# Optimization experiments

Hardware: AMD Instinct MI355X
Metric: run time of the kernel (lower is better)

The kernel has to match this reference:

```python
import jax, jax.numpy as jnp
import numpy as np
from jax import lax

T, B, C = 1024, 64, 512


def setup_inputs() -> dict:
    key = jax.random.key(0)
    ks = jax.random.split(key, 9)
    x = jax.random.normal(ks[0], (T, B, C), dtype=jnp.float32)
    reset = jax.random.uniform(ks[1], (T, B)) < 0.05
    h0 = jax.random.normal(ks[2], (1, B, C), dtype=jnp.float32)
    c0 = jax.random.normal(ks[3], (1, B, C), dtype=jnp.float32)
    s = 1.0 / np.sqrt(C)
    W_ih = jax.random.uniform(ks[4], (4 * C, C), minval=-s, maxval=s, dtype=jnp.float32)
    W_hh = jax.random.uniform(ks[5], (4 * C, C), minval=-s, maxval=s, dtype=jnp.float32)
    b_ih = jax.random.uniform(ks[6], (4 * C,), minval=-s, maxval=s, dtype=jnp.float32)
    b_hh = jax.random.uniform(ks[7], (4 * C,), minval=-s, maxval=s, dtype=jnp.float32)
    return {"x": x, "reset": reset, "h0": h0, "c0": c0,
            "W_ih": W_ih, "W_hh": W_hh, "b_ih": b_ih, "b_hh": b_hh}


def _reset_lstm(x, reset, h0, c0, W_ih, W_hh, b_ih, b_hh):
    # Semantics of Packer + cuDNN LSTM: at each step t, (h,c) are zeroed for
    # batch elements with reset[t]=True (including t=0), then a standard LSTM
    # cell (torch gate order i,f,g,o) is applied.
    # Precompute input projections for all steps: [T,B,4C]
    xg = jnp.einsum('tbc,gc->tbg', x, W_ih) + b_ih + b_hh

    def step(carry, inp):
        h, c = carry                      # [B,C]
        xgt, rt = inp                     # [B,4C], [B]
        keep = jnp.logical_not(rt)[:, None].astype(h.dtype)
        h = h * keep
        c = c * keep
        gates = xgt + h @ W_hh.T          # [B,4C]
        i, f, g, o = jnp.split(gates, 4, axis=-1)
        c = jax.nn.sigmoid(f) * c + jax.nn.sigmoid(i) * jnp.tanh(g)
        h = jax.nn.sigmoid(o) * jnp.tanh(c)
        return (h, c), h

    (hn, cn), ys = lax.scan(step, (h0[0], c0[0]), (xg, reset))
    return ys  # [T,B,C]; module's forward returns y only


def reference(x, reset, h0, c0, W_ih, W_hh, b_ih, b_hh):
    return _reset_lstm(x, reset, h0, c0, W_ih, W_hh, b_ih, b_hh)
```

## Files before the change

### kernel.cpp

```cpp
#include <hip/hip_runtime.h>
#include <math.h>

typedef __attribute__((ext_vector_type(8))) short short8;
typedef __attribute__((ext_vector_type(4))) float f32x4;

#define TSTEPS 1024
#define BATCH  64
#define CDIM   512
#define CAP    256
#define NPH    4

#define HEXW_OFF   0
#define HEXW_BYTES ((size_t)16 * NPH * CAP * 512 * 4)
#define GSEG_OFF   (HEXW_OFF + HEXW_BYTES)
#define GSEG_BYTES ((size_t)65536 * 4)
#define GCNT_OFF   (GSEG_OFF + GSEG_BYTES)
#define GCNT_BYTES (1024 * 4)
#define FLG_OFF    (GCNT_OFF + GCNT_BYTES)
#define FLG_BYTES  (256 * 16 * 4)
#define SEGT_OFF   (FLG_OFF + FLG_BYTES)
#define SEGT_BYTES ((size_t)64 * 1024 * 4)
#define WS_NEED    (SEGT_OFF + SEGT_BYTES)

#define SMEM_BYTES 103424

__device__ __forceinline__ unsigned short f2bf(float x) {
  unsigned u = __builtin_bit_cast(unsigned, x);
  unsigned r = (u + 0x7FFFu + ((u >> 16) & 1u)) >> 16;
  return (unsigned short)r;
}
__device__ __forceinline__ short8 pack8(float4 lo, float4 hi) {
  short8 r;
  r[0] = (short)f2bf(lo.x); r[1] = (short)f2bf(lo.y);
  r[2] = (short)f2bf(lo.z); r[3] = (short)f2bf(lo.w);
  r[4] = (short)f2bf(hi.x); r[5] = (short)f2bf(hi.y);
  r[6] = (short)f2bf(hi.z); r[7] = (short)f2bf(hi.w);
  return r;
}
__device__ __forceinline__ float sigm(float z) { return 1.0f / (1.0f + __expf(-z)); }
__device__ __forceinline__ float tanh_f(float x) {
  return 2.0f / (1.0f + __expf(-2.0f * x)) - 1.0f;
}
__device__ __forceinline__ void backoff(int rnd) {
  if (rnd == 1) __builtin_amdgcn_s_sleep(1);
  else if (rnd == 2) __builtin_amdgcn_s_sleep(2);
  else if (rnd == 3) __builtin_amdgcn_s_sleep(4);
  else if (rnd >= 4) __builtin_amdgcn_s_sleep(8);
}

__device__ __forceinline__ void pollg(const unsigned* flg, int g, int cg,
                                      unsigned tgt, int lane) {
  const int idx = lane & 15;
  int rnd = 0;
  while (true) {
    unsigned v = (idx == cg)
                     ? 0xffffffffu
                     : __hip_atomic_load(&flg[(g * 16 + idx) * 16],
                                         __ATOMIC_RELAXED, __HIP_MEMORY_SCOPE_AGENT);
    if (__all((int)(v >= tgt))) break;
    backoff(++rnd > 8 ? 8 : rnd);
  }
  asm volatile("" ::: "memory");
}

__global__ __launch_bounds__(512) void seg_setup(const void* __restrict__ rst,
    unsigned* __restrict__ GSEG, unsigned* __restrict__ GCNT,
    unsigned* __restrict__ SEGT) {
  __shared__ unsigned long long RM[1024];
  __shared__ unsigned long long BM[64][17];
  __shared__ unsigned hist[1025], GCl[1025], cur[1025];
  __shared__ unsigned nsegb[64];
  __shared__ int s_oki, s_okf, s_oddnz;
  const int tid = threadIdx.x, lane = tid & 63, wv = tid >> 6;
  if (tid == 0) { s_oki = 1; s_okf = 1; s_oddnz = 0; }
  __syncthreads();
  {
    int oki = 1, okf = 1, oddnz = 0;
    for (int i = tid; i < 1024; i += 512) {
      unsigned v = ((const unsigned*)rst)[i];
      oki &= (v <= 1u);
      okf &= (v == 0u || v == 0x3F800000u);
      if ((i & 1) && v != 0u) oddnz = 1;
    }
    if (!oki) atomicAnd(&s_oki, 0);
    if (!okf) atomicAnd(&s_okf, 0);
    if (oddnz) atomicOr(&s_oddnz, 1);
  }
  __syncthreads();
  const int mode = s_oki ? (s_oddnz ? 0 : 3) : (s_okf ? 2 : 1);
  for (int tt = wv; tt < 1024; tt += 8) {
    int idx = tt * BATCH + lane;
    bool r;
    if (mode == 0)      r = ((const int*)rst)[idx] != 0;
    else if (mode == 1) r = ((const unsigned char*)rst)[idx] != 0;
    else if (mode == 2) r = ((const float*)rst)[idx] != 0.0f;
    else                r = ((const int*)rst)[2 * idx] != 0;
    unsigned long long bm = __ballot((int)r);
    if (lane == 0) RM[tt] = bm;
  }
  for (int i = tid; i < 1025; i += 512) { hist[i] = 0; cur[i] = 0; }
  __syncthreads();
  for (int idx = wv; idx < 1024; idx += 8) {
    int b = idx >> 4, w = idx & 15;
    unsigned long long bit = (RM[w * 64 + lane] >> b) & 1ull;
    unsigned long long m = __ballot((int)(bit != 0ull));
    if (lane == 0) BM[b][w] = m;
  }
  __syncthreads();
  if (tid < 64) {
    int b = tid; unsigned cnt = 0; int s = 0;
    unsigned seed0 = (BM[b][0] & 1ull) ? 0u : 1u;
    for (int w = 0; w < 16; ++w) {
      unsigned long long m = BM[b][w];
      if (w == 0) m &= ~1ull;
      while (m) {
        int t = w * 64 + __builtin_ctzll(m);
        m &= m - 1;
        unsigned len = (unsigned)(t - s);
        unsigned sd = (s == 0) ? seed0 : 0u;
        SEGT[b * 1024 + cnt++] =
            (len << 17) | ((unsigned)s << 7) | ((unsigned)b << 1) | sd;
        atomicAdd(&hist[len], 1u);
        s = t;
      }
    }
    { unsigned len = (unsigned)(1024 - s);
      unsigned sd = (s == 0) ? seed0 : 0u;
      SEGT[b * 1024 + cnt++] =
          (len << 17) | ((unsigned)s << 7) | ((unsigned)b << 1) | sd;
      atomicAdd(&hist[len], 1u); }
    nsegb[b] = cnt;
  }
  __syncthreads();
  if (tid == 0) {
    unsigned acc = 0;
    for (int r = 1023; r >= 0; --r) { acc += hist[r + 1]; GCl[r] = acc; }
    GCl[1024] = 0;
  }
  __syncthreads();
  if (tid < 64) {
    int b = tid;
    for (unsigned k = 0; k < nsegb[b]; ++k) {
      unsigned v = SEGT[b * 1024 + k];
      unsigned len = v >> 17;
      unsigned p = GCl[len] + atomicAdd(&cur[len], 1u);
      GSEG[p] = v;
    }
  }
  __syncthreads();
  for (int i = tid; i < 1024; i += 512) GCNT[i] = GCl[i];
}

__global__ __launch_bounds__(512, 1) void rlstm_seq(
    const float* __restrict__ x, const float* __restrict__ h0,
    const float* __restrict__ c0, const float* __restrict__ whh,
    const float* __restrict__ wih, const float* __restrict__ bih,
    const float* __restrict__ bhh, float* __restrict__ y,
    unsigned* __restrict__ hexw, unsigned* __restrict__ flg,
    const unsigned* __restrict__ GSEG, const unsigned* __restrict__ GCNT) {
  extern __shared__ __align__(16) char smem[];
  float* CSEG = (float*)(smem + 65536);
  unsigned* GC = (unsigned*)(smem + 98304);
  unsigned* SEGL = (unsigned*)(smem + 102400);

  const int tid = threadIdx.x, bid = blockIdx.x;
  const int g = bid >> 4, cg = bid & 15;
  const int lane = tid & 63, wv = tid >> 6;
  const int grp = lane >> 4, lr = lane & 15;
  const int gt = lr >> 2, j = lr & 3;
  const int lcol = wv * 4 + j;
  const int cglob = cg * 32 + lcol;
  const int nglob = gt * CDIM + cglob;
  const int srow = 2 * wv + (lane >> 5);
  const int wcol = lane & 31;
  const int swz = (srow & 7) << 4;

  short8 wfrag[16], wfrag2[16];
#pragma unroll
  for (int kk = 0; kk < 16; ++kk) {
    const float* s = whh + (size_t)nglob * CDIM + kk * 32 + grp * 8;
    float4 lo = *(const float4*)s, hi = *(const float4*)(s + 4);
    wfrag[kk] = pack8(lo, hi);
    const float* s2 = wih + (size_t)nglob * CDIM + kk * 32 + grp * 8;
    float4 lo2 = *(const float4*)s2, hi2 = *(const float4*)(s2 + 4);
    wfrag2[kk] = pack8(lo2, hi2);
  }
  const float bsum = bih[nglob] + bhh[nglob];

  for (int i = tid; i < 1024; i += 512) GC[i] = GCNT[i];
  __syncthreads();

  const unsigned G0 = GC[0];
  const unsigned totg = (G0 > (unsigned)g) ? ((G0 - g + 15u) >> 4) : 0u;
  const int nchunks = (int)((totg + CAP - 1) / CAP);
  unsigned tg = 0, fv = 0;

  for (int chunk = 0; chunk < nchunks; ++chunk) {
    const unsigned cb = (unsigned)chunk * CAP;
    int M0;
    { unsigned t2 = totg;
      M0 = (t2 > cb) ? (int)((t2 - cb > CAP) ? CAP : (t2 - cb)) : 0; }
    if (M0 == 0) break;
    if (chunk > 0) pollg(flg, g, cg, fv, lane);

    ++tg;
    for (int i = tid >> 4; i < M0; i += 32) {
      int c2 = (tid & 15) * 2;
      unsigned sv = GSEG[(size_t)(cb + i) * 16 + g];
      if ((tid & 15) == 0) SEGL[i] = sv;
      int b = (sv >> 1) & 63;
      float ha = 0.f, hb = 0.f, ca = 0.f, cbv = 0.f;
      if (sv & 1u) {
        const float* hp = h0 + (size_t)b * CDIM + cg * 32 + c2;
        ha = hp[0]; hb = hp[1];
        const float* cp = c0 + (size_t)b * CDIM + cg * 32 + c2;
        ca = cp[0]; cbv = cp[1];
      }
      CSEG[i * 32 + c2] = ca; CSEG[i * 32 + c2 + 1] = cbv;
      unsigned lo = ((unsigned)f2bf(ha) << 16) | tg;
      unsigned hi2 = ((unsigned)f2bf(hb) << 16) | tg;
      unsigned long long w = ((unsigned long long)hi2 << 32) | lo;
      __hip_atomic_store((unsigned long long*)hexw +
                             ((size_t)(g * NPH + 0) * CAP + i) * 256 + cg * 16 +
                             (tid & 15),
                         w, __ATOMIC_RELAXED, __HIP_MEMORY_SCOPE_AGENT);
    }
    __syncthreads();

    for (int r = 0;; ++r) {
      if (r >= 1024) break;
      int M;
      { unsigned Gr = GC[r];
        unsigned t2 = (Gr > (unsigned)g) ? ((Gr - g + 15u) >> 4) : 0u;
        M = (t2 > cb) ? (int)((t2 - cb > CAP) ? CAP : (t2 - cb)) : 0; }
      if (M == 0) break;
      int Mn = 0;
      if (r + 1 < 1024) {
        unsigned Gn = GC[r + 1];
        unsigned t2 = (Gn > (unsigned)g) ? ((Gn - g + 15u) >> 4) : 0u;
        Mn = (t2 > cb) ? (int)((t2 - cb > CAP) ? CAP : (t2 - cb)) : 0;
      }
      const int ph = r & (NPH - 1), phw = (r + 1) & (NPH - 1);
      const unsigned wtg = tg + 1;
      unsigned* const wbase = hexw + (size_t)(g * NPH + phw) * CAP * 512;

      for (int i0 = 0; i0 < M; i0 += 16) {
        const int p = ((i0 >> 4) + r) & 1;
        { int i = i0 + srow;
          if (i < M) {
            unsigned sv = SEGL[i];
            int b = (sv >> 1) & 63, s0 = (sv >> 7) & 1023;
            const float* xr = x + ((size_t)(s0 + r) * BATCH + b) * CDIM;
            char* xabuf = smem + 32768 + p * 16384;
#pragma unroll
            for (int k2 = 0; k2 < 2; ++k2) {
              int pp = wcol + 32 * k2;
              float4 lo = *(const float4*)(xr + pp * 8);
              float4 hi = *(const float4*)(xr + pp * 8 + 4);
              *(short8*)(xabuf + srow * 1024 + ((pp * 16) ^ swz)) = pack8(lo, hi);
            }
          }
        }
        char* habuf = smem + p * 16384;
        { int i = i0 + srow;
          if (i < M) {
            const unsigned long long* hq = (const unsigned long long*)hexw +
                ((size_t)(g * NPH + ph) * CAP + i) * 256;
            unsigned long long v8[8];
            unsigned pn = 0xffu;
            int rnd = 0;
            do {
              backoff(rnd > 4 ? 4 : rnd);
              ++rnd;
#pragma unroll
              for (int k = 0; k < 8; ++k)
                if (pn & (1u << k))
                  v8[k] = __hip_atomic_load(hq + wcol + 32 * k, __ATOMIC_RELAXED,
                                            __HIP_MEMORY_SCOPE_AGENT);
              unsigned np = 0;
#pragma unroll
              for (int k = 0; k < 8; ++k) {
                unsigned lo = (unsigned)v8[k];
                unsigned hi = (unsigned)(v8[k] >> 32);
                if (((lo ^ tg) | (hi ^ tg)) & 0xffffu) np |= 1u << k;
              }
              pn = np;
            } while (__any((int)pn));
#pragma unroll
            for (int k = 0; k < 8; ++k) {
              unsigned lo = (unsigned)v8[k];
              unsigned hi = (unsigned)(v8[k] >> 32);
              unsigned pk = (lo >> 16) | (hi & 0xffff0000u);
              int m = wcol + 32 * k;
              *(unsigned*)(habuf + srow * 1024 + ((m * 4) ^ swz)) = pk;
            }
          }
        }
        __syncthreads();

        char* xabuf = smem + 32768 + p * 16384;
        f32x4 h0a = {0.f,0.f,0.f,0.f}, h1a = {0.f,0.f,0.f,0.f};
        f32x4 x0a = {0.f,0.f,0.f,0.f}, x1a = {0.f,0.f,0.f,0.f};
#pragma unroll
        for (int kk = 0; kk < 16; ++kk) {
          const int aoff = ((kk * 64 + grp * 16) ^ ((lr & 7) << 4));
          short8 a = *(const short8*)(habuf + lr * 1024 + aoff);
          short8 ax = *(const short8*)(xabuf + lr * 1024 + aoff);
          if (kk & 1) {
            h1a = __builtin_amdgcn_mfma_f32_16x16x32_bf16(a, wfrag[kk], h1a, 0, 0, 0);
            x1a = __builtin_amdgcn_mfma_f32_16x16x32_bf16(ax, wfrag2[kk], x1a, 0, 0, 0);
          } else {
            h0a = __builtin_amdgcn_mfma_f32_16x16x32_bf16(a, wfrag[kk], h0a, 0, 0, 0);
            x0a = __builtin_amdgcn_mfma_f32_16x16x32_bf16(ax, wfrag2[kk], x0a, 0, 0, 0);
          }
        }
        f32x4 acc = (h0a + h1a) + (x0a + x1a);

        float a0 = acc[0] + bsum, a1 = acc[1] + bsum;
        float a2 = acc[2] + bsum, a3 = acc[3] + bsum;
        const int b0 = gt & 1, b1 = (gt >> 1) & 1;
        float sA0 = b0 ? a0 : a1;
        float sA1 = b0 ? a2 : a3;
        float rA0 = __shfl_xor(sA0, 4);
        float rA1 = __shfl_xor(sA1, 4);
        float k0 = b0 ? a1 : a0;
        float k1 = b0 ? a3 : a2;
        float sB0 = b1 ? k0 : k1;
        float sB1 = b1 ? rA0 : rA1;
        float rB0 = __shfl_xor(sB0, 8);
        float rB1 = __shfl_xor(sB1, 8);
        float m0 = b1 ? k1 : k0;
        float m1 = b1 ? rA1 : rA0;
        float gi = (gt == 0) ? m0 : (gt == 1) ? m1 : (gt == 2) ? rB0 : rB1;
        float gf = (gt == 1) ? m0 : (gt == 0) ? m1 : (gt == 3) ? rB0 : rB1;
        float gg = (gt == 2) ? m0 : (gt == 3) ? m1 : (gt == 0) ? rB0 : rB1;
        float go = (gt == 3) ? m0 : (gt == 2) ? m1 : (gt == 1) ? rB0 : rB1;

        const int i = i0 + grp * 4 + gt;
        if (i < M) {
          float cprev = CSEG[i * 32 + lcol];
          float cn = sigm(gf) * cprev + sigm(gi) * tanh_f(gg);
          CSEG[i * 32 + lcol] = cn;
          float hsel = sigm(go) * tanh_f(cn);
          if (i < Mn) {
            unsigned w = ((unsigned)f2bf(hsel) << 16) | wtg;
            __hip_atomic_store(wbase + (size_t)i * 512 + cglob, w,
                               __ATOMIC_RELAXED, __HIP_MEMORY_SCOPE_AGENT);
          }
          unsigned sv = SEGL[i];
          int rowm = (int)((((sv >> 7) & 1023) + r) * BATCH + ((sv >> 1) & 63));
          y[(size_t)rowm * CDIM + cglob] = hsel;
        }
      }
      ++tg;
    }

    ++fv;
    asm volatile("s_waitcnt vmcnt(0)" ::: "memory");
    __syncthreads();
    if (tid == 0)
      __hip_atomic_store(&flg[(g * 16 + cg) * 16], fv, __ATOMIC_RELAXED,
                         __HIP_MEMORY_SCOPE_AGENT);
  }
}

extern "C" void kernel_launch(void* const* d_in, const int* in_sizes, int n_in,
                              void* d_out, int out_size, void* d_ws, size_t ws_size,
                              hipStream_t stream) {
  (void)in_sizes; (void)n_in; (void)out_size;
  const float* x = (const float*)d_in[0];
  const void* rstp = (const void*)d_in[1];
  const float* h0 = (const float*)d_in[2];
  const float* c0 = (const float*)d_in[3];
  const float* wih = (const float*)d_in[4];
  const float* whh = (const float*)d_in[5];
  const float* bih = (const float*)d_in[6];
  const float* bhh = (const float*)d_in[7];
  float* y = (float*)d_out;

  if (ws_size < WS_NEED) return;

  unsigned* hexw = (unsigned*)((char*)d_ws + HEXW_OFF);
  unsigned* GSEG = (unsigned*)((char*)d_ws + GSEG_OFF);
  unsigned* GCNT = (unsigned*)((char*)d_ws + GCNT_OFF);
  unsigned* flg = (unsigned*)((char*)d_ws + FLG_OFF);
  unsigned* SEGT = (unsigned*)((char*)d_ws + SEGT_OFF);

  (void)hipMemsetAsync(d_ws, 0, FLG_OFF + FLG_BYTES, stream);

  seg_setup<<<dim3(1), dim3(512), 0, stream>>>(rstp, GSEG, GCNT, SEGT);

  (void)hipFuncSetAttribute(reinterpret_cast<const void*>(rlstm_seq),
                            hipFuncAttributeMaxDynamicSharedMemorySize, SMEM_BYTES);
  void* args[] = {(void*)&x,    (void*)&h0,  (void*)&c0,   (void*)&whh,
                  (void*)&wih,  (void*)&bih, (void*)&bhh,  (void*)&y,
                  (void*)&hexw, (void*)&flg, (void*)&GSEG, (void*)&GCNT};
  (void)hipLaunchCooperativeKernel((void*)rlstm_seq, dim3(256), dim3(512), args,
                                   SMEM_BYTES, stream);
}
```

Measured before the change: 1.362 ms.

## Prefetch next x tile into registers and shorten spin backoff

Loads of the next tile's x rows from global memory are issued into registers right after the barrier, so they overlap the MFMA work, and are packed into LDS at the start of the next iteration. This hides global-load latency on the serial recurrence path. The full __syncthreads is replaced by a raw s_barrier that waits only on LDS counters, and the polling backoff sleeps are capped lower to reduce wake-up latency. The changes add register pressure and more polling traffic, and depend on in-flight global loads not needing to complete before the barrier.

```diff
diff --git a/kernel.cpp b/kernel.cpp
--- a/kernel.cpp
+++ b/kernel.cpp
@@ -43,9 +43,13 @@
 }
 __device__ __forceinline__ void backoff(int rnd) {
   if (rnd == 1) __builtin_amdgcn_s_sleep(1);
-  else if (rnd == 2) __builtin_amdgcn_s_sleep(2);
-  else if (rnd == 3) __builtin_amdgcn_s_sleep(4);
-  else if (rnd >= 4) __builtin_amdgcn_s_sleep(8);
+  else if (rnd >= 2) __builtin_amdgcn_s_sleep(2);
+}
+__device__ __forceinline__ void soft_barrier() {
+  __builtin_amdgcn_sched_barrier(0);
+  asm volatile("s_waitcnt lgkmcnt(0)" ::: "memory");
+  __builtin_amdgcn_s_barrier();
+  __builtin_amdgcn_sched_barrier(0);
 }
 
 __device__ __forceinline__ void pollg(const unsigned* flg, int g, int cg,
@@ -58,7 +62,7 @@
                      : __hip_atomic_load(&flg[(g * 16 + idx) * 16],
                                          __ATOMIC_RELAXED, __HIP_MEMORY_SCOPE_AGENT);
     if (__all((int)(v >= tgt))) break;
-    backoff(++rnd > 8 ? 8 : rnd);
+    backoff(++rnd > 2 ? 2 : rnd);
   }
   asm volatile("" ::: "memory");
 }
@@ -194,6 +198,7 @@
   const unsigned totg = (G0 > (unsigned)g) ? ((G0 - g + 15u) >> 4) : 0u;
   const int nchunks = (int)((totg + CAP - 1) / CAP);
   unsigned tg = 0, fv = 0;
+  float4 xv[4] = {{0,0,0,0},{0,0,0,0},{0,0,0,0},{0,0,0,0}};
 
   for (int chunk = 0; chunk < nchunks; ++chunk) {
     const unsigned cb = (unsigned)chunk * CAP;
@@ -227,6 +232,18 @@
     }
     __syncthreads();
 
+    { int i = srow;
+      if (i < M0) {
+        unsigned sv = SEGL[i];
+        int b = (sv >> 1) & 63, s0 = (sv >> 7) & 1023;
+        const float* xr = x + ((size_t)s0 * BATCH + b) * CDIM;
+        xv[0] = *(const float4*)(xr + wcol * 8);
+        xv[1] = *(const float4*)(xr + wcol * 8 + 4);
+        xv[2] = *(const float4*)(xr + (wcol + 32) * 8);
+        xv[3] = *(const float4*)(xr + (wcol + 32) * 8 + 4);
+      }
+    }
+
     for (int r = 0;; ++r) {
       if (r >= 1024) break;
       int M;
@@ -246,22 +263,17 @@
 
       for (int i0 = 0; i0 < M; i0 += 16) {
         const int p = ((i0 >> 4) + r) & 1;
+        char* habuf = smem + p * 16384;
+        char* xabuf = smem + 32768 + p * 16384;
+
         { int i = i0 + srow;
           if (i < M) {
-            unsigned sv = SEGL[i];
-            int b = (sv >> 1) & 63, s0 = (sv >> 7) & 1023;
-            const float* xr = x + ((size_t)(s0 + r) * BATCH + b) * CDIM;
-            char* xabuf = smem + 32768 + p * 16384;
-#pragma unroll
-            for (int k2 = 0; k2 < 2; ++k2) {
-              int pp = wcol + 32 * k2;
-              float4 lo = *(const float4*)(xr + pp * 8);
-              float4 hi = *(const float4*)(xr + pp * 8 + 4);
-              *(short8*)(xabuf + srow * 1024 + ((pp * 16) ^ swz)) = pack8(lo, hi);
-            }
+            *(short8*)(xabuf + srow * 1024 + ((wcol * 16) ^ swz)) =
+                pack8(xv[0], xv[1]);
+            *(short8*)(xabuf + srow * 1024 + (((wcol + 32) * 16) ^ swz)) =
+                pack8(xv[2], xv[3]);
           }
         }
-        char* habuf = smem + p * 16384;
         { int i = i0 + srow;
           if (i < M) {
             const unsigned long long* hq = (const unsigned long long*)hexw +
@@ -270,7 +282,7 @@
             unsigned pn = 0xffu;
             int rnd = 0;
             do {
-              backoff(rnd > 4 ? 4 : rnd);
+              backoff(rnd > 2 ? 2 : rnd);
               ++rnd;
 #pragma unroll
               for (int k = 0; k < 8; ++k)
@@ -296,9 +308,22 @@
             }
           }
         }
-        __syncthreads();
-
-        char* xabuf = smem + 32768 + p * 16384;
+        soft_barrier();
+
+        { int nii = i0 + 16, nbound = M, nr = r;
+          if (nii >= M) { nii = 0; nbound = Mn; nr = r + 1; }
+          int i = nii + srow;
+          if (i < nbound) {
+            unsigned sv = SEGL[i];
+            int b = (sv >> 1) & 63, s0 = (sv >> 7) & 1023;
+            const float* xr = x + ((size_t)(s0 + nr) * BATCH + b) * CDIM;
+            xv[0] = *(const float4*)(xr + wcol * 8);
+            xv[1] = *(const float4*)(xr + wcol * 8 + 4);
+            xv[2] = *(const float4*)(xr + (wcol + 32) * 8);
+            xv[3] = *(const float4*)(xr + (wcol + 32) * 8 + 4);
+          }
+        }
+
         f32x4 h0a = {0.f,0.f,0.f,0.f}, h1a = {0.f,0.f,0.f,0.f};
         f32x4 x0a = {0.f,0.f,0.f,0.f}, x1a = {0.f,0.f,0.f,0.f};
 #pragma unroll
```

Result: faster. 1.207 ms (-11.4%).
